# Kernel tuning notes

Measured on AMD Instinct MI355X. Metric: run time of the kernel, lower is better.

Reference implementation:

```python
import jax, jax.numpy as jnp
import numpy as np

# Faithful RBF layer math:
# dists[n,k] = sum_d relu(sigma[d]) * (x[n,d]-center[k,d])^2  (original builds an NxN
# matrix per center just to take its diagonal; we use the algebraic expansion
# x^2.s - 2 (x*s).c^T + c^2.s which is O(N*K*D) and identical math)
# D2 = 1 - dists * relu(width); concat bias column of ones; out = D2_bias @ relu(W_out)

N, D, K, OUT = 131072, 256, 256, 128

def setup_inputs() -> dict:
    key = jax.random.key(0)
    k1, k2, k3, k4 = jax.random.split(key, 4)
    x = jax.random.normal(k1, (N, D), dtype=jnp.float32)
    # 'uniform' keras initializer ~ U(-0.05, 0.05)
    center = jax.random.uniform(k2, (K, D), minval=-0.05, maxval=0.05, dtype=jnp.float32)
    sigma = jax.random.uniform(k3, (1, D), minval=0.5, maxval=1.0, dtype=jnp.float32)
    width = jnp.ones((1, K), dtype=jnp.float32)
    output_weights = jax.random.uniform(k4, (1 + K, OUT), minval=0.5, maxval=1.0, dtype=jnp.float32)
    return {"x": x, "center": center, "sigma": sigma, "width": width,
            "output_weights": output_weights}

def reference(x, center, sigma, width, output_weights):
    s = jax.nn.relu(sigma[0])                       # [D]
    x2 = (x * x) @ s                                # [N]
    c2 = (center * center) @ s                      # [K]
    cross = (x * s) @ center.T                      # [N,K]
    dists = x2[:, None] - 2.0 * cross + c2[None, :] # [N,K] weighted sq-dists
    D2 = 1.0 - dists * jax.nn.relu(width)           # [N,K]
    ones = jnp.ones((x.shape[0], 1), dtype=x.dtype)
    D2_bias = jnp.concatenate([ones, D2], axis=1)   # [N,1+K]
    return D2_bias @ jax.nn.relu(output_weights)    # [N,OUT]
```

## Files before the change

kernel.cpp:

```cpp
#include <hip/hip_runtime.h>


typedef short  short8 __attribute__((ext_vector_type(8)));
typedef __bf16 bf16x8 __attribute__((ext_vector_type(8)));
typedef float  f32x4  __attribute__((ext_vector_type(4)));

#define N_ 131072
#define D_ 256
#define K_ 256
#define O_ 128

__device__ __forceinline__ unsigned short f2bf_bits(float f) {
  unsigned u = __builtin_bit_cast(unsigned, f);
  u += 0x7fffu + ((u >> 16) & 1u);
  return (unsigned short)(u >> 16);
}

__device__ __forceinline__ float relu(float v) { return v > 0.f ? v : 0.f; }

__global__ __launch_bounds__(256) void rbf_pre(
    const float* __restrict__ center, const float* __restrict__ sigma,
    const float* __restrict__ width,  const float* __restrict__ W,
    short* __restrict__ Mfrag, float* __restrict__ Bo, float* __restrict__ S1)
{
  const int tid = threadIdx.x;
  if (blockIdx.x < 64) {
    const int ot = blockIdx.x & 7;
    const int ks = blockIdx.x >> 3;
    __shared__ float ww[K_][16];
    __shared__ float cen[K_][32];
#pragma unroll
    for (int i = 0; i < 16; ++i) {
      const int k  = i * 16 + (tid >> 4);
      const int oc = tid & 15;
      ww[k][oc] = relu(width[k]) * relu(W[(1 + k) * O_ + ot * 16 + oc]);
    }
#pragma unroll
    for (int i = 0; i < 32; ++i) {
      const int k  = i * 8 + (tid >> 5);
      const int dc = tid & 31;
      cen[k][dc] = center[k * D_ + ks * 32 + dc];
    }
    __syncthreads();
    const int j   = tid & 7;
    const int lf  = tid >> 3;
    const int oc  = lf & 15;
    const int dc1 = (lf >> 4) * 8 + j;
    float a1 = 0.f, a2 = 0.f;
#pragma unroll 8
    for (int k = 0; k < K_; ++k) {
      const float w = ww[k][oc];
      a1 = fmaf(cen[k][dc1],      w, a1);
      a2 = fmaf(cen[k][dc1 + 16], w, a2);
    }
    const int e1 = blockIdx.x * 512 + tid;
    const int d1 = ks * 32 + dc1;
    Mfrag[e1]       = (short)f2bf_bits(a1 * relu(sigma[d1]));
    Mfrag[e1 + 256] = (short)f2bf_bits(a2 * relu(sigma[d1 + 16]));
  } else {
    __shared__ float c2s[K_];
    {
      const int k = tid;
      float acc = 0.f;
      for (int d = 0; d < D_; ++d) {
        const float c = center[k * D_ + d];
        acc = fmaf(c * c, relu(sigma[d]), acc);
      }
      c2s[k] = acc;
    }
    __syncthreads();
    if (tid < O_) {
      const int o = tid;
      float s1 = 0.f, sum = 0.f, c2w = 0.f;
      for (int k = 0; k < K_; ++k) {
        const float w  = relu(width[k]);
        const float wr = relu(W[(1 + k) * O_ + o]);
        s1  = fmaf(w, wr, s1);
        sum += wr;
        c2w = fmaf(c2s[k] * w, wr, c2w);
      }
      Bo[o] = relu(W[o]) + sum - c2w;
      S1[o] = s1;
    }
  }
}

__global__ __launch_bounds__(256, 2) void rbf_main(
    const float* __restrict__ x, const float* __restrict__ sigma,
    const short* __restrict__ Mfrag, const float* __restrict__ Bo,
    const float* __restrict__ S1, float* __restrict__ out)
{
  const int lane = threadIdx.x & 63;
  const int wv   = threadIdx.x >> 6;
  const int m    = lane & 15;
  const int q    = lane >> 4;
  const long rowBase = ((long)blockIdx.x * 4 + wv) * 32;

  const float* xr0 = x + (rowBase + m) * D_ + q * 8;
  const float* xr1 = xr0 + 16 * D_;

  f32x4 raw0[16], raw1[16];
#pragma unroll
  for (int ks = 0; ks < 8; ++ks) {
    raw0[ks * 2]     = *(const f32x4*)(xr0 + ks * 32);
    raw0[ks * 2 + 1] = *(const f32x4*)(xr0 + ks * 32 + 4);
  }
#pragma unroll
  for (int ks = 0; ks < 8; ++ks) {
    raw1[ks * 2]     = *(const f32x4*)(xr1 + ks * 32);
    raw1[ks * 2 + 1] = *(const f32x4*)(xr1 + ks * 32 + 4);
  }

  const float* sp = sigma + q * 8;
  bf16x8 a0[8], a1[8];
  float x20 = 0.f, x21 = 0.f;
#pragma unroll
  for (int ks = 0; ks < 8; ++ks) {
    float sv[8], v0[8], v1[8];
    *(f32x4*)(sv)     = *(const f32x4*)(sp + ks * 32);
    *(f32x4*)(sv + 4) = *(const f32x4*)(sp + ks * 32 + 4);
    *(f32x4*)(v0)     = raw0[ks * 2];
    *(f32x4*)(v0 + 4) = raw0[ks * 2 + 1];
    *(f32x4*)(v1)     = raw1[ks * 2];
    *(f32x4*)(v1 + 4) = raw1[ks * 2 + 1];
    short8 b0, b1;
#pragma unroll
    for (int jj = 0; jj < 8; ++jj) {
      const float s = relu(sv[jj]);
      x20 = fmaf(s * v0[jj], v0[jj], x20);
      x21 = fmaf(s * v1[jj], v1[jj], x21);
      b0[jj] = (short)f2bf_bits(v0[jj]);
      b1[jj] = (short)f2bf_bits(v1[jj]);
    }
    a0[ks] = __builtin_bit_cast(bf16x8, b0);
    a1[ks] = __builtin_bit_cast(bf16x8, b1);
  }
  x20 += __shfl_xor(x20, 16);  x20 += __shfl_xor(x20, 32);
  x21 += __shfl_xor(x21, 16);  x21 += __shfl_xor(x21, 32);

  float bo[8], s1v[8];
#pragma unroll
  for (int ot = 0; ot < 8; ++ot) {
    bo[ot]  = Bo[ot * 16 + m];
    s1v[ot] = S1[ot * 16 + m];
  }

  const short8* Mf = (const short8*)Mfrag;
#pragma unroll
  for (int ot = 0; ot < 8; ++ot) {
    f32x4 acc0 = {0.f, 0.f, 0.f, 0.f};
    f32x4 acc1 = {0.f, 0.f, 0.f, 0.f};
#pragma unroll
    for (int ks = 0; ks < 8; ++ks) {
      const short8 bs = Mf[(ks * 8 + ot) * 64 + lane];
      const bf16x8 bb = __builtin_bit_cast(bf16x8, bs);
      acc0 = __builtin_amdgcn_mfma_f32_16x16x32_bf16(a0[ks], bb, acc0, 0, 0, 0);
      acc1 = __builtin_amdgcn_mfma_f32_16x16x32_bf16(a1[ks], bb, acc1, 0, 0, 0);
    }
    const int o = ot * 16 + m;
    float* op0 = out + rowBase * O_ + o;
    float* op1 = op0 + 16 * O_;
#pragma unroll
    for (int r = 0; r < 4; ++r) {
      const int rr = q * 4 + r;
      const float x2r0 = __shfl(x20, rr);
      const float x2r1 = __shfl(x21, rr);
      __builtin_nontemporal_store(
          fmaf(2.f, acc0[r], fmaf(-x2r0, s1v[ot], bo[ot])), op0 + (long)rr * O_);
      __builtin_nontemporal_store(
          fmaf(2.f, acc1[r], fmaf(-x2r1, s1v[ot], bo[ot])), op1 + (long)rr * O_);
    }
  }
}

extern "C" void kernel_launch(void* const* d_in, const int* in_sizes, int n_in,
                              void* d_out, int out_size, void* d_ws, size_t ws_size,
                              hipStream_t stream) {
  (void)in_sizes; (void)n_in; (void)out_size; (void)ws_size;
  const float* x      = (const float*)d_in[0];
  const float* center = (const float*)d_in[1];
  const float* sigma  = (const float*)d_in[2];
  const float* width  = (const float*)d_in[3];
  const float* W      = (const float*)d_in[4];
  float* out = (float*)d_out;

  short* Mfrag = (short*)d_ws;
  float* Bo    = (float*)((char*)d_ws + 65536);
  float* S1    = (float*)((char*)d_ws + 66048);

  hipLaunchKernelGGL(rbf_pre, dim3(65), dim3(256), 0, stream,
                     center, sigma, width, W, Mfrag, Bo, S1);
  hipLaunchKernelGGL(rbf_main, dim3(1024), dim3(256), 0, stream,
                     x, sigma, Mfrag, Bo, S1, out);
}
```

Measured before the change: 260.4 us.

## Stage projection matrix in LDS and loop 16-row tiles per wave

The main kernel now loads the whole 64KB bf16 B fragment matrix into shared memory once per 512-thread block. Each wave then processes two 16-row tiles in a loop instead of two 16-row halves at once, which roughly halves live registers. This removes repeated global/L2 reads of B and targets higher occupancy via launch bounds (512,3). Nontemporal stores are replaced with plain stores, and Bo/S1 are reloaded per output tile. The 64KB of LDS per block may limit how many blocks fit per CU.

```diff
diff --git a/kernel.cpp b/kernel.cpp
--- a/kernel.cpp
+++ b/kernel.cpp
@@ -85,90 +85,81 @@
   }
 }
 
-__global__ __launch_bounds__(256, 2) void rbf_main(
+__global__ __launch_bounds__(512, 3) void rbf_main(
     const float* __restrict__ x, const float* __restrict__ sigma,
     const short* __restrict__ Mfrag, const float* __restrict__ Bo,
     const float* __restrict__ S1, float* __restrict__ out)
 {
-  const int lane = threadIdx.x & 63;
-  const int wv   = threadIdx.x >> 6;
+  __shared__ short8 Blds[4096];
+  const int tid = threadIdx.x;
+  {
+    const short8* Mf8 = (const short8*)Mfrag;
+#pragma unroll
+    for (int i = 0; i < 8; ++i)
+      Blds[i * 512 + tid] = Mf8[i * 512 + tid];
+  }
+
+  const int lane = tid & 63;
+  const int wv   = tid >> 6;
   const int m    = lane & 15;
   const int q    = lane >> 4;
-  const long rowBase = ((long)blockIdx.x * 4 + wv) * 32;
+  const int gw   = blockIdx.x * 8 + wv;
 
-  const float* xr0 = x + (rowBase + m) * D_ + q * 8;
-  const float* xr1 = xr0 + 16 * D_;
+  __syncthreads();
 
-  f32x4 raw0[16], raw1[16];
-#pragma unroll
-  for (int ks = 0; ks < 8; ++ks) {
-    raw0[ks * 2]     = *(const f32x4*)(xr0 + ks * 32);
-    raw0[ks * 2 + 1] = *(const f32x4*)(xr0 + ks * 32 + 4);
-  }
-#pragma unroll
-  for (int ks = 0; ks < 8; ++ks) {
-    raw1[ks * 2]     = *(const f32x4*)(xr1 + ks * 32);
-    raw1[ks * 2 + 1] = *(const f32x4*)(xr1 + ks * 32 + 4);
-  }
+  for (int it = 0; it < 2; ++it) {
+    const long tile    = (long)gw + (long)it * 4096;
+    const long rowBase = tile * 16;
+    const float* xr = x + (rowBase + m) * D_ + q * 8;
 
-  const float* sp = sigma + q * 8;
-  bf16x8 a0[8], a1[8];
-  float x20 = 0.f, x21 = 0.f;
-#pragma unroll
-  for (int ks = 0; ks < 8; ++ks) {
-    float sv[8], v0[8], v1[8];
-    *(f32x4*)(sv)     = *(const f32x4*)(sp + ks * 32);
-    *(f32x4*)(sv + 4) = *(const f32x4*)(sp + ks * 32 + 4);
-    *(f32x4*)(v0)     = raw0[ks * 2];
-    *(f32x4*)(v0 + 4) = raw0[ks * 2 + 1];
-    *(f32x4*)(v1)     = raw1[ks * 2];
-    *(f32x4*)(v1 + 4) = raw1[ks * 2 + 1];
-    short8 b0, b1;
-#pragma unroll
-    for (int jj = 0; jj < 8; ++jj) {
-      const float s = relu(sv[jj]);
-      x20 = fmaf(s * v0[jj], v0[jj], x20);
-      x21 = fmaf(s * v1[jj], v1[jj], x21);
-      b0[jj] = (short)f2bf_bits(v0[jj]);
-      b1[jj] = (short)f2bf_bits(v1[jj]);
-    }
-    a0[ks] = __builtin_bit_cast(bf16x8, b0);
-    a1[ks] = __builtin_bit_cast(bf16x8, b1);
-  }
-  x20 += __shfl_xor(x20, 16);  x20 += __shfl_xor(x20, 32);
-  x21 += __shfl_xor(x21, 16);  x21 += __shfl_xor(x21, 32);
-
-  float bo[8], s1v[8];
-#pragma unroll
-  for (int ot = 0; ot < 8; ++ot) {
-    bo[ot]  = Bo[ot * 16 + m];
-    s1v[ot] = S1[ot * 16 + m];
-  }
-
-  const short8* Mf = (const short8*)Mfrag;
-#pragma unroll
-  for (int ot = 0; ot < 8; ++ot) {
-    f32x4 acc0 = {0.f, 0.f, 0.f, 0.f};
-    f32x4 acc1 = {0.f, 0.f, 0.f, 0.f};
+    f32x4 raw[16];
 #pragma unroll
     for (int ks = 0; ks < 8; ++ks) {
-      const short8 bs = Mf[(ks * 8 + ot) * 64 + lane];
-      const bf16x8 bb = __builtin_bit_cast(bf16x8, bs);
-      acc0 = __builtin_amdgcn_mfma_f32_16x16x32_bf16(a0[ks], bb, acc0, 0, 0, 0);
-      acc1 = __builtin_amdgcn_mfma_f32_16x16x32_bf16(a1[ks], bb, acc1, 0, 0, 0);
+      raw[2 * ks]     = *(const f32x4*)(xr + ks * 32);
+      raw[2 * ks + 1] = *(const f32x4*)(xr + ks * 32 + 4);
     }
-    const int o = ot * 16 + m;
-    float* op0 = out + rowBase * O_ + o;
-    float* op1 = op0 + 16 * O_;
+
+    const float* sp = sigma + q * 8;
+    bf16x8 a[8];
+    float x2 = 0.f;
 #pragma unroll
-    for (int r = 0; r < 4; ++r) {
-      const int rr = q * 4 + r;
-      const float x2r0 = __shfl(x20, rr);
-      const float x2r1 = __shfl(x21, rr);
-      __builtin_nontemporal_store(
-          fmaf(2.f, acc0[r], fmaf(-x2r0, s1v[ot], bo[ot])), op0 + (long)rr * O_);
-      __builtin_nontemporal_store(
-          fmaf(2.f, acc1[r], fmaf(-x2r1, s1v[ot], bo[ot])), op1 + (long)rr * O_);
+    for (int ks = 0; ks < 8; ++ks) {
+      float sv[8], v[8];
+      *(f32x4*)(sv)     = *(const f32x4*)(sp + ks * 32);
+      *(f32x4*)(sv + 4) = *(const f32x4*)(sp + ks * 32 + 4);
+      *(f32x4*)(v)      = raw[2 * ks];
+      *(f32x4*)(v + 4)  = raw[2 * ks + 1];
+      short8 ab;
+#pragma unroll
+      for (int jj = 0; jj < 8; ++jj) {
+        const float s = relu(sv[jj]);
+        x2 = fmaf(s * v[jj], v[jj], x2);
+        ab[jj] = (short)f2bf_bits(v[jj]);
+      }
+      a[ks] = __builtin_bit_cast(bf16x8, ab);
+    }
+    x2 += __shfl_xor(x2, 16);
+    x2 += __shfl_xor(x2, 32);
+
+#pragma unroll
+    for (int ot = 0; ot < 8; ++ot) {
+      f32x4 acc = {0.f, 0.f, 0.f, 0.f};
+#pragma unroll
+      for (int ks = 0; ks < 8; ++ks) {
+        const bf16x8 bb =
+            __builtin_bit_cast(bf16x8, Blds[(ks * 8 + ot) * 64 + lane]);
+        acc = __builtin_amdgcn_mfma_f32_16x16x32_bf16(a[ks], bb, acc, 0, 0, 0);
+      }
+      const int   o  = ot * 16 + m;
+      const float bo = Bo[o];
+      const float s1 = S1[o];
+      float* op = out + rowBase * O_ + o;
+#pragma unroll
+      for (int r = 0; r < 4; ++r) {
+        const int rr = q * 4 + r;
+        const float x2r = __shfl(x2, rr);
+        op[(long)rr * O_] = fmaf(2.f, acc[r], fmaf(-x2r, s1, bo));
+      }
     }
   }
 }
@@ -190,6 +181,6 @@
 
   hipLaunchKernelGGL(rbf_pre, dim3(65), dim3(256), 0, stream,
                      center, sigma, width, W, Mfrag, Bo, S1);
-  hipLaunchKernelGGL(rbf_main, dim3(1024), dim3(256), 0, stream,
+  hipLaunchKernelGGL(rbf_main, dim3(512), dim3(512), 0, stream,
                      x, sigma, Mfrag, Bo, S1, out);
 }
```

New measurement: 481.5 us. +84.9%, slower.
